# Kernel tuning notes

Hardware: AMD Instinct MI355X
Metric: run time of the kernel (lower is better)

Reference implementation:

```python
import jax, jax.numpy as jnp
import numpy as np

N_NODES = 100000
N_EDGES = 1600000
VOCAB = 10000
HIDDEN = 128
EMB1 = 128
EMB2 = 128
L1 = 64
N_GRAPHS = 256


def setup_inputs() -> dict:
    key = jax.random.key(0)
    ks = jax.random.split(key, 16)
    inp = {
        "x": jax.random.randint(ks[0], (N_NODES,), 0, VOCAB, dtype=jnp.int32),
        "edge_index": jax.random.randint(ks[1], (2, N_EDGES), 0, N_NODES, dtype=jnp.int32),
        "edge_weight": jax.random.uniform(ks[2], (N_EDGES,), dtype=jnp.float32),
        "batch": jnp.sort(jax.random.randint(ks[3], (N_NODES,), 0, N_GRAPHS, dtype=jnp.int32)),
        # parameters
        "emb_w": jax.random.normal(ks[4], (VOCAB, HIDDEN), dtype=jnp.float32) * 0.5,
        "w1_rel": jax.random.normal(ks[5], (EMB1, HIDDEN), dtype=jnp.float32) * (HIDDEN ** -0.5),
        "b1_rel": jnp.zeros((EMB1,), dtype=jnp.float32),
        "w1_root": jax.random.normal(ks[6], (EMB1, HIDDEN), dtype=jnp.float32) * (HIDDEN ** -0.5),
        "w2_rel": jax.random.normal(ks[7], (EMB2, EMB1), dtype=jnp.float32) * (EMB1 ** -0.5),
        "b2_rel": jnp.zeros((EMB2,), dtype=jnp.float32),
        "w2_root": jax.random.normal(ks[8], (EMB2, EMB1), dtype=jnp.float32) * (EMB1 ** -0.5),
        "cls1_w": jax.random.normal(ks[9], (L1, EMB2), dtype=jnp.float32) * (EMB2 ** -0.5),
        "cls1_b": jnp.zeros((L1,), dtype=jnp.float32),
        "cls2_w": jax.random.normal(ks[10], (2, L1), dtype=jnp.float32) * (L1 ** -0.5),
        "cls2_b": jnp.zeros((2,), dtype=jnp.float32),
    }
    return inp


def _embedding_max_norm(emb_w, idx, max_norm=1.0):
    # torch Embedding(max_norm=1): looked-up rows are renormalized to norm <= 1
    rows = emb_w[idx]                                        # [N, H]
    norm = jnp.linalg.norm(rows, axis=-1, keepdims=True)
    scale = jnp.minimum(1.0, max_norm / (norm + 1e-7))
    return rows * scale


def _graph_conv(h, src, dst, ew, w_rel, b_rel, w_root):
    # PyG GraphConv: out = lin_rel(sum_{j->i} w_ji * x_j) + lin_root(x_i)
    msg = h[src] * ew[:, None]                               # [E, D] gather
    agg = jax.ops.segment_sum(msg, dst, num_segments=N_NODES)  # [N, D] scatter-add
    return agg @ w_rel.T + b_rel + h @ w_root.T


def reference(x, edge_index, edge_weight, batch, emb_w,
              w1_rel, b1_rel, w1_root, w2_rel, b2_rel, w2_root,
              cls1_w, cls1_b, cls2_w, cls2_b):
    src, dst = edge_index[0], edge_index[1]
    h = _embedding_max_norm(emb_w, x)                        # [N, HIDDEN]
    # dropout is identity in eval mode
    h = jax.nn.relu(_graph_conv(h, src, dst, edge_weight, w1_rel, b1_rel, w1_root))
    h = jax.nn.relu(_graph_conv(h, src, dst, edge_weight, w2_rel, b2_rel, w2_root))
    # global mean pool over graphs
    sums = jax.ops.segment_sum(h, batch, num_segments=N_GRAPHS)        # [G, EMB2]
    counts = jax.ops.segment_sum(jnp.ones((h.shape[0],), h.dtype), batch,
                                 num_segments=N_GRAPHS)
    pooled = sums / jnp.maximum(counts, 1.0)[:, None]
    z = jax.nn.relu(pooled @ cls1_w.T + cls1_b)
    z = z @ cls2_w.T + cls2_b
    return jax.nn.softmax(z, axis=1)                          # [G, 2]
```

## Files before the change

kernel.cpp:

```cpp
#include <hip/hip_runtime.h>
#include <stdint.h>

#define NN 100000
#define NE 1600000
#define NG 256
#define NB 196
#define CHUNK 4096
#define NCH 391

typedef __attribute__((ext_vector_type(8))) short bf16x8;
typedef __attribute__((ext_vector_type(4))) float f32x4;

__device__ inline uint32_t f2bf(float f){
    uint32_t u = __float_as_uint(f);
    return (u + 0x7FFFu + ((u >> 16) & 1u)) >> 16;
}
__device__ inline float bflo(uint32_t u){ return __uint_as_float(u << 16); }
__device__ inline float bfhi(uint32_t u){ return __uint_as_float(u & 0xFFFF0000u); }
__device__ inline float bf1(short s){ return __uint_as_float(((uint32_t)(uint16_t)s) << 16); }

__global__ __launch_bounds__(256) void k_embed(const int* __restrict__ x,
                                               const float* __restrict__ emb,
                                               uint32_t* __restrict__ hout,
                                               int* __restrict__ bcnt){
    int idx = blockIdx.x * 256 + threadIdx.x;
    if (idx < NB) bcnt[idx] = 0;
    int w = threadIdx.x >> 6, l = threadIdx.x & 63;
    int n = blockIdx.x * 4 + w;
    int r = x[n];
    const float2* e2 = (const float2*)emb;
    float2 v = e2[(size_t)r * 64 + l];
    float ss = v.x * v.x + v.y * v.y;
    #pragma unroll
    for (int off = 32; off; off >>= 1) ss += __shfl_xor(ss, off, 64);
    float sc = fminf(1.f, 1.f / (sqrtf(ss) + 1e-7f));
    hout[(size_t)n * 64 + l] = f2bf(v.x * sc) | (f2bf(v.y * sc) << 16);
}

__global__ __launch_bounds__(256) void k_pack(const float* __restrict__ w1rel, const float* __restrict__ w1root,
                                              const float* __restrict__ w2rel, const float* __restrict__ w2root,
                                              short* __restrict__ wf){
    int id = blockIdx.x * 256 + threadIdx.x;
    int i = id & 7, lane = (id >> 3) & 63, ks = (id >> 9) & 3, j0 = (id >> 11) & 7, m = id >> 14;
    const float* W = (m == 0) ? w1rel : (m == 1) ? w1root : (m == 2) ? w2rel : w2root;
    int j = j0 * 16 + (lane & 15);
    int k = ks * 32 + (lane >> 4) * 8 + i;
    wf[id] = (short)f2bf(W[j * 128 + k]);
}

__global__ __launch_bounds__(256) void k_bhist(const int* __restrict__ edst, int* __restrict__ bcnt){
    __shared__ int lh[NB];
    int t = threadIdx.x;
    int c0 = blockIdx.x * CHUNK;
    int cnt = min(CHUNK, NE - c0);
    if (t < NB) lh[t] = 0;
    __syncthreads();
    for (int i = t; i < cnt; i += 256) atomicAdd(&lh[edst[c0 + i] >> 9], 1);
    __syncthreads();
    if (t < NB && lh[t]) atomicAdd(&bcnt[t], lh[t]);
}

__global__ __launch_bounds__(256) void k_bscan(const int* __restrict__ bcnt,
                                               int* __restrict__ bbase, int* __restrict__ bfill,
                                               int* __restrict__ ptrA){
    __shared__ int sc[256];
    int t = threadIdx.x;
    int v = (t < NB) ? bcnt[t] : 0;
    sc[t] = v; __syncthreads();
    for (int off = 1; off < 256; off <<= 1){
        int u = (t >= off) ? sc[t - off] : 0;
        __syncthreads();
        sc[t] += u;
        __syncthreads();
    }
    if (t < NB){ bbase[t] = sc[t] - v; bfill[t] = 0; }
    if (t == 0){ bbase[NB] = NE; ptrA[NN] = NE; }
}

__global__ __launch_bounds__(256) void k_bscatter(const int* __restrict__ esrc, const int* __restrict__ edst,
                                                  const float* __restrict__ ew,
                                                  const int* __restrict__ bbase, int* __restrict__ bfill,
                                                  uint2* __restrict__ cse2){
    __shared__ uint2 rec[CHUNK];
    __shared__ unsigned char slotb[CHUNK];
    __shared__ int hist[NB], start[NB], gbase[NB], sc[256];
    int t = threadIdx.x;
    int c0 = blockIdx.x * CHUNK;
    int cnt = min(CHUNK, NE - c0);
    if (t < NB) hist[t] = 0;
    __syncthreads();
    for (int i = t; i < cnt; i += 256) atomicAdd(&hist[edst[c0 + i] >> 9], 1);
    __syncthreads();
    int v = (t < NB) ? hist[t] : 0;
    sc[t] = v; __syncthreads();
    for (int off = 1; off < 256; off <<= 1){
        int u = (t >= off) ? sc[t - off] : 0;
        __syncthreads();
        sc[t] += u;
        __syncthreads();
    }
    if (t < NB){
        start[t] = sc[t] - v;
        if (v > 0) gbase[t] = bbase[t] + atomicAdd(&bfill[t], v);
    }
    __syncthreads();
    if (t < NB) hist[t] = 0;
    __syncthreads();
    for (int i = t; i < cnt; i += 256){
        int d = edst[c0 + i];
        int b = d >> 9;
        int slot = start[b] + atomicAdd(&hist[b], 1);
        rec[slot] = make_uint2((uint32_t)esrc[c0 + i] | ((uint32_t)(d & 511) << 23),
                               __float_as_uint(ew[c0 + i]));
        slotb[slot] = (unsigned char)b;
    }
    __syncthreads();
    for (int i = t; i < cnt; i += 256){
        int b = slotb[i];
        cse2[gbase[b] + (i - start[b])] = rec[i];
    }
}

__global__ __launch_bounds__(256) void k_bcsr(const uint2* __restrict__ cse2,
                                              const int* __restrict__ bbase,
                                              int* __restrict__ ptrA,
                                              uint2* __restrict__ cse){
    __shared__ int cnt[512], sc[512], st[512];
    int t = threadIdx.x;
    int b = blockIdx.x;
    int ebase = bbase[b], eend = bbase[b + 1];
    int nb = b << 9;
    cnt[t] = 0; cnt[t + 256] = 0;
    __syncthreads();
    for (int i = ebase + t; i < eend; i += 256){
        uint2 r = cse2[i];
        atomicAdd(&cnt[r.x >> 23], 1);
    }
    __syncthreads();
    sc[t] = cnt[t]; sc[t + 256] = cnt[t + 256];
    __syncthreads();
    for (int off = 1; off < 512; off <<= 1){
        int v0 = (t >= off) ? sc[t - off] : 0;
        int v1 = sc[t + 256 - off];
        __syncthreads();
        sc[t] += v0; sc[t + 256] += v1;
        __syncthreads();
    }
    st[t] = sc[t] - cnt[t];
    st[t + 256] = sc[t + 256] - cnt[t + 256];
    if (nb + t < NN)       ptrA[nb + t]       = ebase + st[t];
    if (nb + 256 + t < NN) ptrA[nb + 256 + t] = ebase + st[t + 256];
    cnt[t] = 0; cnt[t + 256] = 0;
    __syncthreads();
    for (int i = ebase + t; i < eend; i += 256){
        uint2 r = cse2[i];
        int dr = r.x >> 23;
        int pos = st[dr] + atomicAdd(&cnt[dr], 1);
        cse[ebase + pos] = make_uint2(r.x & 0x7FFFFFu, r.y);
    }
}

__global__ __launch_bounds__(256) void k_gstart(const int* __restrict__ batch, int* __restrict__ gstart, int N){
    int i = blockIdx.x * 256 + threadIdx.x;
    if (i > N) return;
    int bprev = (i == 0) ? -1 : batch[i - 1];
    int bcur  = (i == N) ? NG : batch[i];
    for (int g = bprev + 1; g <= bcur; ++g) gstart[g] = i;
}

__global__ __launch_bounds__(256) void k_agg(const uint32_t* __restrict__ hin,
                                             uint32_t* __restrict__ aggo,
                                             const int* __restrict__ ptr,
                                             const uint2* __restrict__ cse){
    int w = threadIdx.x >> 6, l = threadIdx.x & 63;
    int n = blockIdx.x * 4 + w;
    int p0 = ptr[n], p1 = ptr[n + 1];
    float ax0 = 0, ay0 = 0, ax1 = 0, ay1 = 0, ax2 = 0, ay2 = 0, ax3 = 0, ay3 = 0;
    int e = p0;
    for (; e + 4 <= p1; e += 4){
        uint2 r0 = cse[e], r1 = cse[e + 1], r2 = cse[e + 2], r3 = cse[e + 3];
        uint32_t v0 = hin[(size_t)r0.x * 64 + l];
        uint32_t v1 = hin[(size_t)r1.x * 64 + l];
        uint32_t v2 = hin[(size_t)r2.x * 64 + l];
        uint32_t v3 = hin[(size_t)r3.x * 64 + l];
        float w0 = __uint_as_float(r0.y), w1 = __uint_as_float(r1.y);
        float w2 = __uint_as_float(r2.y), w3 = __uint_as_float(r3.y);
        ax0 += w0 * bflo(v0); ay0 += w0 * bfhi(v0);
        ax1 += w1 * bflo(v1); ay1 += w1 * bfhi(v1);
        ax2 += w2 * bflo(v2); ay2 += w2 * bfhi(v2);
        ax3 += w3 * bflo(v3); ay3 += w3 * bfhi(v3);
    }
    for (; e < p1; ++e){
        uint2 r0 = cse[e];
        uint32_t v0 = hin[(size_t)r0.x * 64 + l];
        float w0 = __uint_as_float(r0.y);
        ax0 += w0 * bflo(v0); ay0 += w0 * bfhi(v0);
    }
    float ax = (ax0 + ax1) + (ax2 + ax3);
    float ay = (ay0 + ay1) + (ay2 + ay3);
    aggo[(size_t)n * 64 + l] = f2bf(ax) | (f2bf(ay) << 16);
}

__global__ __launch_bounds__(256) void k_gemm(const short* __restrict__ hin,
                                              const short* __restrict__ agg,
                                              short* __restrict__ hout,
                                              const bf16x8* __restrict__ wrel,
                                              const bf16x8* __restrict__ wroot,
                                              const float* __restrict__ bias){
    int t = threadIdx.x, w = t >> 6, l = t & 63;
    int rbase = blockIdx.x * 128 + w * 32;
    int r0 = rbase + (l & 15);
    int rA0 = min(r0, NN - 1);
    int rA1 = min(r0 + 16, NN - 1);
    int kb = (l >> 4) * 8;

    bf16x8 aA[2][4], aH[2][4];
    const short* pa0 = agg + (size_t)rA0 * 128 + kb;
    const short* pa1 = agg + (size_t)rA1 * 128 + kb;
    const short* ph0 = hin + (size_t)rA0 * 128 + kb;
    const short* ph1 = hin + (size_t)rA1 * 128 + kb;
    #pragma unroll
    for (int ks = 0; ks < 4; ++ks){
        aA[0][ks] = *(const bf16x8*)(pa0 + ks * 32);
        aA[1][ks] = *(const bf16x8*)(pa1 + ks * 32);
        aH[0][ks] = *(const bf16x8*)(ph0 + ks * 32);
        aH[1][ks] = *(const bf16x8*)(ph1 + ks * 32);
    }

    for (int j0 = 0; j0 < 8; ++j0){
        f32x4 acc0 = {0.f, 0.f, 0.f, 0.f}, acc1 = {0.f, 0.f, 0.f, 0.f};
        #pragma unroll
        for (int ks = 0; ks < 4; ++ks){
            bf16x8 br = wrel [(j0 * 4 + ks) * 64 + l];
            bf16x8 bo = wroot[(j0 * 4 + ks) * 64 + l];
            acc0 = __builtin_amdgcn_mfma_f32_16x16x32_bf16(aA[0][ks], br, acc0, 0, 0, 0);
            acc0 = __builtin_amdgcn_mfma_f32_16x16x32_bf16(aH[0][ks], bo, acc0, 0, 0, 0);
            acc1 = __builtin_amdgcn_mfma_f32_16x16x32_bf16(aA[1][ks], br, acc1, 0, 0, 0);
            acc1 = __builtin_amdgcn_mfma_f32_16x16x32_bf16(aH[1][ks], bo, acc1, 0, 0, 0);
        }
        int col = j0 * 16 + (l & 15);
        float bv = bias[col];
        int rb = rbase + (l >> 4) * 4;
        #pragma unroll
        for (int r = 0; r < 4; ++r){
            int row = rb + r;
            if (row < NN){
                float v = fmaxf(acc0[r] + bv, 0.f);
                hout[(size_t)row * 128 + col] = (short)f2bf(v);
            }
            int row1 = rb + 16 + r;
            if (row1 < NN){
                float v = fmaxf(acc1[r] + bv, 0.f);
                hout[(size_t)row1 * 128 + col] = (short)f2bf(v);
            }
        }
    }
}

__global__ __launch_bounds__(128) void k_pool(const short* __restrict__ h,
                                              const int* __restrict__ gstart,
                                              float* __restrict__ pooled){
    int g = blockIdx.x, f = threadIdx.x;
    int s = gstart[g], e = gstart[g + 1];
    float a0 = 0, a1 = 0, a2 = 0, a3 = 0;
    int i = s;
    for (; i + 3 < e; i += 4){
        a0 += bf1(h[(size_t)i * 128 + f]);
        a1 += bf1(h[(size_t)(i + 1) * 128 + f]);
        a2 += bf1(h[(size_t)(i + 2) * 128 + f]);
        a3 += bf1(h[(size_t)(i + 3) * 128 + f]);
    }
    for (; i < e; ++i) a0 += bf1(h[(size_t)i * 128 + f]);
    float sum = (a0 + a1) + (a2 + a3);
    int cnt = e - s;
    pooled[g * 128 + f] = sum / fmaxf((float)cnt, 1.f);
}

__global__ __launch_bounds__(64) void k_cls(const float* __restrict__ pooled,
                                            const float* __restrict__ c1w, const float* __restrict__ c1b,
                                            const float* __restrict__ c2w, const float* __restrict__ c2b,
                                            float* __restrict__ out){
    __shared__ float pl[128];
    __shared__ float z[64];
    __shared__ float logits[2];
    int g = blockIdx.x, t = threadIdx.x;
    pl[t] = pooled[g * 128 + t];
    pl[t + 64] = pooled[g * 128 + 64 + t];
    __syncthreads();
    float acc = c1b[t];
    #pragma unroll 4
    for (int k = 0; k < 128; ++k) acc += pl[k] * c1w[t * 128 + k];
    z[t] = fmaxf(acc, 0.f);
    __syncthreads();
    if (t < 2){
        float a = c2b[t];
        for (int k = 0; k < 64; ++k) a += z[k] * c2w[t * 64 + k];
        logits[t] = a;
    }
    __syncthreads();
    if (t == 0){
        float m = fmaxf(logits[0], logits[1]);
        float e0 = expf(logits[0] - m), e1 = expf(logits[1] - m);
        float s = e0 + e1;
        out[g * 2 + 0] = e0 / s;
        out[g * 2 + 1] = e1 / s;
    }
}

extern "C" void kernel_launch(void* const* d_in, const int* in_sizes, int n_in,
                              void* d_out, int out_size, void* d_ws, size_t ws_size,
                              hipStream_t stream) {
    const int*   x      = (const int*)  d_in[0];
    const int*   eidx   = (const int*)  d_in[1];
    const float* ew     = (const float*)d_in[2];
    const int*   batch  = (const int*)  d_in[3];
    const float* emb    = (const float*)d_in[4];
    const float* w1rel  = (const float*)d_in[5];
    const float* b1     = (const float*)d_in[6];
    const float* w1root = (const float*)d_in[7];
    const float* w2rel  = (const float*)d_in[8];
    const float* b2     = (const float*)d_in[9];
    const float* w2root = (const float*)d_in[10];
    const float* c1w    = (const float*)d_in[11];
    const float* c1b    = (const float*)d_in[12];
    const float* c2w    = (const float*)d_in[13];
    const float* c2b    = (const float*)d_in[14];
    float* out = (float*)d_out;

    const int N = NN;
    const int E = NE;

    char* p = (char*)d_ws;
    auto alloc = [&](size_t bytes) -> void* {
        void* r = (void*)p;
        p += (bytes + 255) & ~(size_t)255;
        return r;
    };
    uint32_t* hA   = (uint32_t*)alloc((size_t)N * 64 * 4);
    uint32_t* hB   = (uint32_t*)alloc((size_t)N * 64 * 4);
    uint32_t* agg  = (uint32_t*)alloc((size_t)N * 64 * 4);
    int*   ptrA   = (int*)  alloc((size_t)(N + 1) * 4);
    int*   bcnt   = (int*)  alloc(NB * 4);
    int*   bbase  = (int*)  alloc((NB + 1) * 4);
    int*   bfill  = (int*)  alloc(NB * 4);
    uint2* cse2   = (uint2*)alloc((size_t)E * 8);
    uint2* cse    = (uint2*)alloc((size_t)E * 8);
    int*   gstart = (int*)  alloc((NG + 1) * 4);
    float* pooled = (float*)alloc((size_t)NG * 128 * 4);
    short* wf     = (short*)alloc(4 * 16384 * 2);
    (void)alloc(65536);

    const bf16x8* wf1rel  = (const bf16x8*)(wf);
    const bf16x8* wf1root = (const bf16x8*)(wf + 16384);
    const bf16x8* wf2rel  = (const bf16x8*)(wf + 32768);
    const bf16x8* wf2root = (const bf16x8*)(wf + 49152);

    const int* esrc = eidx;
    const int* edst = eidx + E;

    k_embed<<<N / 4, 256, 0, stream>>>(x, emb, hA, bcnt);
    k_pack <<<256, 256, 0, stream>>>(w1rel, w1root, w2rel, w2root, wf);

    k_bhist   <<<NCH, 256, 0, stream>>>(edst, bcnt);
    k_bscan   <<<1,   256, 0, stream>>>(bcnt, bbase, bfill, ptrA);
    k_bscatter<<<NCH, 256, 0, stream>>>(esrc, edst, ew, bbase, bfill, cse2);
    k_bcsr    <<<NB,  256, 0, stream>>>(cse2, bbase, ptrA, cse);
    k_gstart  <<<(N + 1 + 255) / 256, 256, 0, stream>>>(batch, gstart, N);

    int ngemm = (N + 127) / 128;
    k_agg <<<N / 4, 256, 0, stream>>>(hA, agg, ptrA, cse);
    k_gemm<<<ngemm, 256, 0, stream>>>((const short*)hA, (const short*)agg, (short*)hB,
                                      wf1rel, wf1root, b1);
    k_agg <<<N / 4, 256, 0, stream>>>(hB, agg, ptrA, cse);
    k_gemm<<<ngemm, 256, 0, stream>>>((const short*)hB, (const short*)agg, (short*)hA,
                                      wf2rel, wf2root, b2);

    k_pool<<<NG, 128, 0, stream>>>((const short*)hA, gstart, pooled);
    k_cls<<<NG, 64, 0, stream>>>(pooled, c1w, c1b, c2w, c2b, out);
}
```

Measured before the change: 405.0 us.

## Fuse preprocessing kernels, merge pool+classifier, and split agg wave across two edges

Merges embedding, destination histogram and graph-start computation into one heterogeneous launch, and moves the bcnt zeroing into the pack kernel. Pool and classifier are fused into one kernel, which removes the pooled buffer. The aggregation kernel now has each half-wave handle a different edge with 8-byte loads per lane, then combines the halves with a cross-lane shuffle. This cuts launch count and raises memory-level parallelism in the gather. The cost is some idle lanes in the tail loop and extra shuffle work.

```diff
diff --git a/kernel.cpp b/kernel.cpp
--- a/kernel.cpp
+++ b/kernel.cpp
@@ -7,6 +7,7 @@
 #define NB 196
 #define CHUNK 4096
 #define NCH 391
+#define NGS 392
 
 typedef __attribute__((ext_vector_type(8))) short bf16x8;
 typedef __attribute__((ext_vector_type(4))) float f32x4;
@@ -19,28 +20,11 @@
 __device__ inline float bfhi(uint32_t u){ return __uint_as_float(u & 0xFFFF0000u); }
 __device__ inline float bf1(short s){ return __uint_as_float(((uint32_t)(uint16_t)s) << 16); }
 
-__global__ __launch_bounds__(256) void k_embed(const int* __restrict__ x,
-                                               const float* __restrict__ emb,
-                                               uint32_t* __restrict__ hout,
-                                               int* __restrict__ bcnt){
-    int idx = blockIdx.x * 256 + threadIdx.x;
-    if (idx < NB) bcnt[idx] = 0;
-    int w = threadIdx.x >> 6, l = threadIdx.x & 63;
-    int n = blockIdx.x * 4 + w;
-    int r = x[n];
-    const float2* e2 = (const float2*)emb;
-    float2 v = e2[(size_t)r * 64 + l];
-    float ss = v.x * v.x + v.y * v.y;
-    #pragma unroll
-    for (int off = 32; off; off >>= 1) ss += __shfl_xor(ss, off, 64);
-    float sc = fminf(1.f, 1.f / (sqrtf(ss) + 1e-7f));
-    hout[(size_t)n * 64 + l] = f2bf(v.x * sc) | (f2bf(v.y * sc) << 16);
-}
-
 __global__ __launch_bounds__(256) void k_pack(const float* __restrict__ w1rel, const float* __restrict__ w1root,
                                               const float* __restrict__ w2rel, const float* __restrict__ w2root,
-                                              short* __restrict__ wf){
+                                              short* __restrict__ wf, int* __restrict__ bcnt){
     int id = blockIdx.x * 256 + threadIdx.x;
+    if (id < NB) bcnt[id] = 0;
     int i = id & 7, lane = (id >> 3) & 63, ks = (id >> 9) & 3, j0 = (id >> 11) & 7, m = id >> 14;
     const float* W = (m == 0) ? w1rel : (m == 1) ? w1root : (m == 2) ? w2rel : w2root;
     int j = j0 * 16 + (lane & 15);
@@ -48,16 +32,42 @@
     wf[id] = (short)f2bf(W[j * 128 + k]);
 }
 
-__global__ __launch_bounds__(256) void k_bhist(const int* __restrict__ edst, int* __restrict__ bcnt){
-    __shared__ int lh[NB];
-    int t = threadIdx.x;
-    int c0 = blockIdx.x * CHUNK;
-    int cnt = min(CHUNK, NE - c0);
-    if (t < NB) lh[t] = 0;
-    __syncthreads();
-    for (int i = t; i < cnt; i += 256) atomicAdd(&lh[edst[c0 + i] >> 9], 1);
-    __syncthreads();
-    if (t < NB && lh[t]) atomicAdd(&bcnt[t], lh[t]);
+__global__ __launch_bounds__(256) void k_embed(const int* __restrict__ x,
+                                               const float* __restrict__ emb,
+                                               uint32_t* __restrict__ hout,
+                                               const int* __restrict__ edst,
+                                               int* __restrict__ bcnt,
+                                               const int* __restrict__ batch,
+                                               int* __restrict__ gstart){
+    int bid = blockIdx.x;
+    if (bid < NN / 4){
+        int w = threadIdx.x >> 6, l = threadIdx.x & 63;
+        int n = bid * 4 + w;
+        int r = x[n];
+        const float2* e2 = (const float2*)emb;
+        float2 v = e2[(size_t)r * 64 + l];
+        float ss = v.x * v.x + v.y * v.y;
+        #pragma unroll
+        for (int off = 32; off; off >>= 1) ss += __shfl_xor(ss, off, 64);
+        float sc = fminf(1.f, 1.f / (sqrtf(ss) + 1e-7f));
+        hout[(size_t)n * 64 + l] = f2bf(v.x * sc) | (f2bf(v.y * sc) << 16);
+    } else if (bid < NN / 4 + NCH){
+        __shared__ int lh[NB];
+        int t = threadIdx.x;
+        int c0 = (bid - NN / 4) * CHUNK;
+        int cnt = min(CHUNK, NE - c0);
+        if (t < NB) lh[t] = 0;
+        __syncthreads();
+        for (int i = t; i < cnt; i += 256) atomicAdd(&lh[edst[c0 + i] >> 9], 1);
+        __syncthreads();
+        if (t < NB && lh[t]) atomicAdd(&bcnt[t], lh[t]);
+    } else {
+        int i = (bid - NN / 4 - NCH) * 256 + threadIdx.x;
+        if (i > NN) return;
+        int bprev = (i == 0) ? -1 : batch[i - 1];
+        int bcur  = (i == NN) ? NG : batch[i];
+        for (int g = bprev + 1; g <= bcur; ++g) gstart[g] = i;
+    }
 }
 
 __global__ __launch_bounds__(256) void k_bscan(const int* __restrict__ bcnt,
@@ -160,45 +170,66 @@
     }
 }
 
-__global__ __launch_bounds__(256) void k_gstart(const int* __restrict__ batch, int* __restrict__ gstart, int N){
-    int i = blockIdx.x * 256 + threadIdx.x;
-    if (i > N) return;
-    int bprev = (i == 0) ? -1 : batch[i - 1];
-    int bcur  = (i == N) ? NG : batch[i];
-    for (int g = bprev + 1; g <= bcur; ++g) gstart[g] = i;
-}
-
 __global__ __launch_bounds__(256) void k_agg(const uint32_t* __restrict__ hin,
                                              uint32_t* __restrict__ aggo,
                                              const int* __restrict__ ptr,
                                              const uint2* __restrict__ cse){
     int w = threadIdx.x >> 6, l = threadIdx.x & 63;
+    int h = l >> 5, c = l & 31;
     int n = blockIdx.x * 4 + w;
     int p0 = ptr[n], p1 = ptr[n + 1];
-    float ax0 = 0, ay0 = 0, ax1 = 0, ay1 = 0, ax2 = 0, ay2 = 0, ax3 = 0, ay3 = 0;
+    const uint2* hin2 = (const uint2*)hin;
+    float a0 = 0, a1 = 0, a2 = 0, a3 = 0;
+    float b0 = 0, b1 = 0, b2 = 0, b3 = 0;
     int e = p0;
+    for (; e + 8 <= p1; e += 8){
+        uint2 rA0 = cse[e + 2 * h],     rB0 = cse[e + 2 * h + 1];
+        uint2 rA1 = cse[e + 4 + 2 * h], rB1 = cse[e + 4 + 2 * h + 1];
+        uint2 vA0 = hin2[(size_t)rA0.x * 32 + c];
+        uint2 vB0 = hin2[(size_t)rB0.x * 32 + c];
+        uint2 vA1 = hin2[(size_t)rA1.x * 32 + c];
+        uint2 vB1 = hin2[(size_t)rB1.x * 32 + c];
+        float wA0 = __uint_as_float(rA0.y), wB0 = __uint_as_float(rB0.y);
+        float wA1 = __uint_as_float(rA1.y), wB1 = __uint_as_float(rB1.y);
+        a0 += wA0 * bflo(vA0.x); a1 += wA0 * bfhi(vA0.x);
+        a2 += wA0 * bflo(vA0.y); a3 += wA0 * bfhi(vA0.y);
+        b0 += wB0 * bflo(vB0.x); b1 += wB0 * bfhi(vB0.x);
+        b2 += wB0 * bflo(vB0.y); b3 += wB0 * bfhi(vB0.y);
+        a0 += wA1 * bflo(vA1.x); a1 += wA1 * bfhi(vA1.x);
+        a2 += wA1 * bflo(vA1.y); a3 += wA1 * bfhi(vA1.y);
+        b0 += wB1 * bflo(vB1.x); b1 += wB1 * bfhi(vB1.x);
+        b2 += wB1 * bflo(vB1.y); b3 += wB1 * bfhi(vB1.y);
+    }
     for (; e + 4 <= p1; e += 4){
-        uint2 r0 = cse[e], r1 = cse[e + 1], r2 = cse[e + 2], r3 = cse[e + 3];
-        uint32_t v0 = hin[(size_t)r0.x * 64 + l];
-        uint32_t v1 = hin[(size_t)r1.x * 64 + l];
-        uint32_t v2 = hin[(size_t)r2.x * 64 + l];
-        uint32_t v3 = hin[(size_t)r3.x * 64 + l];
-        float w0 = __uint_as_float(r0.y), w1 = __uint_as_float(r1.y);
-        float w2 = __uint_as_float(r2.y), w3 = __uint_as_float(r3.y);
-        ax0 += w0 * bflo(v0); ay0 += w0 * bfhi(v0);
-        ax1 += w1 * bflo(v1); ay1 += w1 * bfhi(v1);
-        ax2 += w2 * bflo(v2); ay2 += w2 * bfhi(v2);
-        ax3 += w3 * bflo(v3); ay3 += w3 * bfhi(v3);
-    }
-    for (; e < p1; ++e){
-        uint2 r0 = cse[e];
-        uint32_t v0 = hin[(size_t)r0.x * 64 + l];
-        float w0 = __uint_as_float(r0.y);
-        ax0 += w0 * bflo(v0); ay0 += w0 * bfhi(v0);
-    }
-    float ax = (ax0 + ax1) + (ax2 + ax3);
-    float ay = (ay0 + ay1) + (ay2 + ay3);
-    aggo[(size_t)n * 64 + l] = f2bf(ax) | (f2bf(ay) << 16);
+        uint2 rA = cse[e + 2 * h], rB = cse[e + 2 * h + 1];
+        uint2 vA = hin2[(size_t)rA.x * 32 + c];
+        uint2 vB = hin2[(size_t)rB.x * 32 + c];
+        float wA = __uint_as_float(rA.y), wB = __uint_as_float(rB.y);
+        a0 += wA * bflo(vA.x); a1 += wA * bfhi(vA.x);
+        a2 += wA * bflo(vA.y); a3 += wA * bfhi(vA.y);
+        b0 += wB * bflo(vB.x); b1 += wB * bfhi(vB.x);
+        b2 += wB * bflo(vB.y); b3 += wB * bfhi(vB.y);
+    }
+    for (; e < p1; e += 2){
+        int idx = e + h;
+        bool act = idx < p1;
+        uint2 r = act ? cse[idx] : make_uint2(0u, 0u);
+        uint2 v = hin2[(size_t)r.x * 32 + c];
+        float wt = act ? __uint_as_float(r.y) : 0.f;
+        a0 += wt * bflo(v.x); a1 += wt * bfhi(v.x);
+        a2 += wt * bflo(v.y); a3 += wt * bfhi(v.y);
+    }
+    a0 += b0; a1 += b1; a2 += b2; a3 += b3;
+    a0 += __shfl_xor(a0, 32, 64);
+    a1 += __shfl_xor(a1, 32, 64);
+    a2 += __shfl_xor(a2, 32, 64);
+    a3 += __shfl_xor(a3, 32, 64);
+    if (h == 0){
+        uint2 o;
+        o.x = f2bf(a0) | (f2bf(a1) << 16);
+        o.y = f2bf(a2) | (f2bf(a3) << 16);
+        ((uint2*)aggo)[(size_t)n * 32 + c] = o;
+    }
 }
 
 __global__ __launch_bounds__(256) void k_gemm(const short* __restrict__ hin,
@@ -257,40 +288,35 @@
     }
 }
 
-__global__ __launch_bounds__(128) void k_pool(const short* __restrict__ h,
-                                              const int* __restrict__ gstart,
-                                              float* __restrict__ pooled){
-    int g = blockIdx.x, f = threadIdx.x;
+__global__ __launch_bounds__(128) void k_poolcls(const short* __restrict__ h,
+                                                 const int* __restrict__ gstart,
+                                                 const float* __restrict__ c1w, const float* __restrict__ c1b,
+                                                 const float* __restrict__ c2w, const float* __restrict__ c2b,
+                                                 float* __restrict__ out){
+    __shared__ float pl[128];
+    __shared__ float z[64];
+    __shared__ float logits[2];
+    int g = blockIdx.x, t = threadIdx.x;
     int s = gstart[g], e = gstart[g + 1];
     float a0 = 0, a1 = 0, a2 = 0, a3 = 0;
     int i = s;
     for (; i + 3 < e; i += 4){
-        a0 += bf1(h[(size_t)i * 128 + f]);
-        a1 += bf1(h[(size_t)(i + 1) * 128 + f]);
-        a2 += bf1(h[(size_t)(i + 2) * 128 + f]);
-        a3 += bf1(h[(size_t)(i + 3) * 128 + f]);
-    }
-    for (; i < e; ++i) a0 += bf1(h[(size_t)i * 128 + f]);
+        a0 += bf1(h[(size_t)i * 128 + t]);
+        a1 += bf1(h[(size_t)(i + 1) * 128 + t]);
+        a2 += bf1(h[(size_t)(i + 2) * 128 + t]);
+        a3 += bf1(h[(size_t)(i + 3) * 128 + t]);
+    }
+    for (; i < e; ++i) a0 += bf1(h[(size_t)i * 128 + t]);
     float sum = (a0 + a1) + (a2 + a3);
     int cnt = e - s;
-    pooled[g * 128 + f] = sum / fmaxf((float)cnt, 1.f);
-}
-
-__global__ __launch_bounds__(64) void k_cls(const float* __restrict__ pooled,
-                                            const float* __restrict__ c1w, const float* __restrict__ c1b,
-                                            const float* __restrict__ c2w, const float* __restrict__ c2b,
-                                            float* __restrict__ out){
-    __shared__ float pl[128];
-    __shared__ float z[64];
-    __shared__ float logits[2];
-    int g = blockIdx.x, t = threadIdx.x;
-    pl[t] = pooled[g * 128 + t];
-    pl[t + 64] = pooled[g * 128 + 64 + t];
-    __syncthreads();
-    float acc = c1b[t];
-    #pragma unroll 4
-    for (int k = 0; k < 128; ++k) acc += pl[k] * c1w[t * 128 + k];
-    z[t] = fmaxf(acc, 0.f);
+    pl[t] = sum / fmaxf((float)cnt, 1.f);
+    __syncthreads();
+    if (t < 64){
+        float acc = c1b[t];
+        #pragma unroll 4
+        for (int k = 0; k < 128; ++k) acc += pl[k] * c1w[t * 128 + k];
+        z[t] = fmaxf(acc, 0.f);
+    }
     __syncthreads();
     if (t < 2){
         float a = c2b[t];
@@ -301,9 +327,9 @@
     if (t == 0){
         float m = fmaxf(logits[0], logits[1]);
         float e0 = expf(logits[0] - m), e1 = expf(logits[1] - m);
-        float s = e0 + e1;
-        out[g * 2 + 0] = e0 / s;
-        out[g * 2 + 1] = e1 / s;
+        float ss = e0 + e1;
+        out[g * 2 + 0] = e0 / ss;
+        out[g * 2 + 1] = e1 / ss;
     }
 }
 
@@ -346,7 +372,6 @@
     uint2* cse2   = (uint2*)alloc((size_t)E * 8);
     uint2* cse    = (uint2*)alloc((size_t)E * 8);
     int*   gstart = (int*)  alloc((NG + 1) * 4);
-    float* pooled = (float*)alloc((size_t)NG * 128 * 4);
     short* wf     = (short*)alloc(4 * 16384 * 2);
     (void)alloc(65536);
 
@@ -358,14 +383,12 @@
     const int* esrc = eidx;
     const int* edst = eidx + E;
 
-    k_embed<<<N / 4, 256, 0, stream>>>(x, emb, hA, bcnt);
-    k_pack <<<256, 256, 0, stream>>>(w1rel, w1root, w2rel, w2root, wf);
-
-    k_bhist   <<<NCH, 256, 0, stream>>>(edst, bcnt);
+    k_pack <<<256, 256, 0, stream>>>(w1rel, w1root, w2rel, w2root, wf, bcnt);
+    k_embed<<<N / 4 + NCH + NGS, 256, 0, stream>>>(x, emb, hA, edst, bcnt, batch, gstart);
+
     k_bscan   <<<1,   256, 0, stream>>>(bcnt, bbase, bfill, ptrA);
     k_bscatter<<<NCH, 256, 0, stream>>>(esrc, edst, ew, bbase, bfill, cse2);
     k_bcsr    <<<NB,  256, 0, stream>>>(cse2, bbase, ptrA, cse);
-    k_gstart  <<<(N + 1 + 255) / 256, 256, 0, stream>>>(batch, gstart, N);
 
     int ngemm = (N + 127) / 128;
     k_agg <<<N / 4, 256, 0, stream>>>(hA, agg, ptrA, cse);
@@ -375,6 +398,5 @@
     k_gemm<<<ngemm, 256, 0, stream>>>((const short*)hB, (const short*)agg, (short*)hA,
                                       wf2rel, wf2root, b2);
 
-    k_pool<<<NG, 128, 0, stream>>>((const short*)hA, gstart, pooled);
-    k_cls<<<NG, 64, 0, stream>>>(pooled, c1w, c1b, c2w, c2b, out);
-}
+    k_poolcls<<<NG, 128, 0, stream>>>((const short*)hA, gstart, c1w, c1b, c2w, c2b, out);
+}
```

After: 377.0 us. 6.9% less time.
